# Optimization experiments

Hardware: AMD Instinct MI355X
Metric: run time of the kernel (lower is better)

Reference implementation:

```python
import jax, jax.numpy as jnp
import numpy as np

SCALE_POS = 2.0
SCALE_NEG = 40.0
THRESH_POS = 0.5
THRESH_NEG = 0.5
MARGIN = 0.1
EPS = 1e-5


def setup_inputs() -> dict:
    key = jax.random.key(0)
    kf, kl = jax.random.split(key)
    B, D, NUM_CLASSES = 4096, 1024, 64
    feats = jax.random.normal(kf, (B, D), dtype=jnp.float32)
    feats = feats / jnp.linalg.norm(feats, axis=1, keepdims=True)  # L2-normalized embeddings
    labels = jax.random.randint(kl, (B,), 0, NUM_CLASSES, dtype=jnp.int64)
    return {"feats": feats, "labels": labels}


def reference(feats, labels):
    B = feats.shape[0]
    sim = jnp.matmul(feats, feats.T)  # [B, B]
    same = labels[:, None] == labels[None, :]
    pos_mask = same & (sim < 1.0 - EPS)  # drop self / near-duplicate pairs
    neg_mask = ~same

    # hard mining: keep negatives above min positive - margin, positives below max negative + margin
    min_pos = jnp.min(jnp.where(pos_mask, sim, jnp.inf), axis=1)   # [B]
    max_neg = jnp.max(jnp.where(neg_mask, sim, -jnp.inf), axis=1)  # [B]
    neg_sel = neg_mask & (sim + MARGIN > min_pos[:, None])
    pos_sel = pos_mask & (sim - MARGIN < max_neg[:, None])

    pos_sum = jnp.sum(jnp.where(pos_sel, jnp.exp(-SCALE_POS * (sim - THRESH_POS)), 0.0), axis=1)
    neg_sum = jnp.sum(jnp.where(neg_sel, jnp.exp(SCALE_NEG * (sim - THRESH_NEG)), 0.0), axis=1)
    pos_loss = jnp.log1p(pos_sum) / SCALE_POS
    neg_loss = jnp.log1p(neg_sum) / SCALE_NEG

    valid = jnp.any(pos_sel, axis=1) & jnp.any(neg_sel, axis=1)  # rows skipped by original loop
    return jnp.sum(jnp.where(valid, pos_loss + neg_loss, 0.0)) / B
```

## Files before the change

### kernel.cpp

```cpp
#include <hip/hip_runtime.h>

typedef _Float16 half8 __attribute__((ext_vector_type(8)));
typedef float floatx4 __attribute__((ext_vector_type(4)));
typedef int intx4 __attribute__((ext_vector_type(4)));
typedef int intx8 __attribute__((ext_vector_type(8)));
typedef __attribute__((address_space(1))) const void gvoid;
typedef __attribute__((address_space(3))) void svoid;

#define SCALE_POS 2.0f
#define SCALE_NEG 40.0f
#define THRESH 0.5f
#define MARGIN 0.1f
#define EPSV 1e-5f

__device__ __forceinline__ unsigned f2ord(float f) {
    unsigned u = __float_as_uint(f);
    return (u & 0x80000000u) ? ~u : (u | 0x80000000u);
}
__device__ __forceinline__ float ord2f(unsigned e) {
    unsigned v = (e & 0x80000000u) ? (e & 0x7fffffffu) : ~e;
    return __uint_as_float(v);
}

#define ORD_POS_INF 0xff800000u
#define ORD_NEG_INF 0x007fffffu

__global__ void k_init(const float* __restrict__ feats,
                       unsigned char* __restrict__ f8,
                       unsigned* __restrict__ minp, unsigned* __restrict__ maxn,
                       float* __restrict__ psum, float* __restrict__ nsum,
                       unsigned* __restrict__ cnts,
                       int total4, int B) {
    int i = blockIdx.x * blockDim.x + threadIdx.x;
    if (i < total4) {
        float4 v = ((const float4*)feats)[i];
        int w = 0;
        w = __builtin_amdgcn_cvt_pk_fp8_f32(v.x, v.y, w, false);
        w = __builtin_amdgcn_cvt_pk_fp8_f32(v.z, v.w, w, true);
        ((int*)f8)[i] = w;
    }
    if (i < B) {
        minp[i] = ORD_POS_INF;
        maxn[i] = ORD_NEG_INF;
        psum[i] = 0.f;
        nsum[i] = 0.f;
    }
    if (i < 2048) cnts[i] = 0;
}

__global__ void __launch_bounds__(128, 2)
k_gemm_h(const unsigned char* __restrict__ f8,
         const int* __restrict__ labels,
         unsigned* __restrict__ minp_ord,
         unsigned* __restrict__ maxn_ord,
         _Float16* __restrict__ simh,
         int D, int nb) {
    __shared__ __align__(16) unsigned char As[128 * 128];
    __shared__ __align__(16) unsigned char Bs[64 * 128];
    __shared__ int labR[128], labC[64];

    const int bid = blockIdx.x;
    int t = bid >> 1;
    const int h = bid & 1;
    int rb = 0, rem = t;
    while (rem >= nb - rb) { rem -= nb - rb; ++rb; }
    const int cb = rb + rem;
    const int rowBase = rb * 128;
    const int colBase = cb * 128 + h * 64;

    const int tid = threadIdx.x;
    const int lane = tid & 63;
    const int wave = tid >> 6;
    const int q = lane >> 4;
    const int cIn = lane & 15;

    labR[tid] = labels[rowBase + tid];
    if (tid < 64) labC[tid] = labels[colBase + tid];

    const int subrow = lane >> 3;
    const int swz = (lane & 7) ^ subrow;
    const unsigned char* gP[12];
    unsigned char* lP[12];
#pragma unroll
    for (int j = 0; j < 12; ++j) {
        const int c = wave * 12 + j;
        const int grow = (c < 16) ? (rowBase + c * 8 + subrow)
                                  : (colBase + (c - 16) * 8 + subrow);
        gP[j] = f8 + (size_t)grow * D + swz * 16;
        lP[j] = ((c < 16) ? (As + c * 1024) : (Bs + (c - 16) * 1024)) + lane * 16;
    }

    int aOff0[4], aOff1[4], bOff0[4], bOff1[4];
#pragma unroll
    for (int i = 0; i < 4; ++i) {
        const int rA = wave * 64 + i * 16 + cIn;
        aOff0[i] = rA * 128 + ((2 * q) ^ (rA & 7)) * 16;
        aOff1[i] = rA * 128 + ((2 * q + 1) ^ (rA & 7)) * 16;
        const int rB = i * 16 + cIn;
        bOff0[i] = rB * 128 + ((2 * q) ^ (rB & 7)) * 16;
        bOff1[i] = rB * 128 + ((2 * q + 1) ^ (rB & 7)) * 16;
    }

    floatx4 acc[4][4] = {};

    const int KT = D >> 7;
    for (int kt = 0; kt < KT; ++kt) {
        const int kOff = kt * 128;
        __syncthreads();
#pragma unroll
        for (int j = 0; j < 12; ++j)
            __builtin_amdgcn_global_load_lds((gvoid*)(gP[j] + kOff), (svoid*)lP[j], 16, 0, 0);
        __syncthreads();

        intx8 a[4], b[4];
#pragma unroll
        for (int i = 0; i < 4; ++i) {
            intx4 lo = *(const intx4*)(As + aOff0[i]);
            intx4 hi = *(const intx4*)(As + aOff1[i]);
            a[i] = __builtin_shufflevector(lo, hi, 0, 1, 2, 3, 4, 5, 6, 7);
        }
#pragma unroll
        for (int i = 0; i < 4; ++i) {
            intx4 lo = *(const intx4*)(Bs + bOff0[i]);
            intx4 hi = *(const intx4*)(Bs + bOff1[i]);
            b[i] = __builtin_shufflevector(lo, hi, 0, 1, 2, 3, 4, 5, 6, 7);
        }
#pragma unroll
        for (int i = 0; i < 4; ++i)
#pragma unroll
            for (int j = 0; j < 4; ++j)
                acc[i][j] = __builtin_amdgcn_mfma_scale_f32_16x16x128_f8f6f4(
                    a[i], b[j], acc[i][j], 0, 0,
                    0, 0x7f7f7f7f,
                    0, 0x7f7f7f7f);
    }

    int rLabv[16];
#pragma unroll
    for (int mi = 0; mi < 4; ++mi)
#pragma unroll
        for (int rr = 0; rr < 4; ++rr)
            rLabv[mi * 4 + rr] = labR[wave * 64 + mi * 16 + q * 4 + rr];
    int cLabv[4];
#pragma unroll
    for (int ni = 0; ni < 4; ++ni)
        cLabv[ni] = labC[ni * 16 + cIn];

    {
        half8* dst = (half8*)(simh + (size_t)bid * 8192 + (size_t)tid * 64);
#pragma unroll
        for (int mi = 0; mi < 4; ++mi) {
            half8 h0, h1;
#pragma unroll
            for (int ni = 0; ni < 2; ++ni)
#pragma unroll
                for (int rr = 0; rr < 4; ++rr) {
                    h0[ni * 4 + rr] = (_Float16)acc[mi][ni][rr];
                    h1[ni * 4 + rr] = (_Float16)acc[mi][ni + 2][rr];
                }
            dst[mi * 2] = h0;
            dst[mi * 2 + 1] = h1;
        }
    }

#pragma unroll
    for (int mi = 0; mi < 4; ++mi)
#pragma unroll
        for (int rr = 0; rr < 4; ++rr) {
            const int rLoc = wave * 64 + mi * 16 + q * 4 + rr;
            const int rLab = rLabv[mi * 4 + rr];
            float vmin = 1e30f, vmax = -1e30f;
#pragma unroll
            for (int ni = 0; ni < 4; ++ni) {
                float s = acc[mi][ni][rr];
                if (rLab == cLabv[ni]) {
                    if (s < 1.0f - EPSV) vmin = fminf(vmin, s);
                } else {
                    vmax = fmaxf(vmax, s);
                }
            }
#pragma unroll
            for (int off = 8; off; off >>= 1) {
                vmin = fminf(vmin, __shfl_xor(vmin, off, 16));
                vmax = fmaxf(vmax, __shfl_xor(vmax, off, 16));
            }
            if (cIn == 0) {
                if (vmin < 1e30f) atomicMin(&minp_ord[rowBase + rLoc], f2ord(vmin));
                if (vmax > -1e30f) atomicMax(&maxn_ord[rowBase + rLoc], f2ord(vmax));
            }
        }

    if (rb != cb) {
#pragma unroll
        for (int ni = 0; ni < 4; ++ni) {
            const int cLab = cLabv[ni];
            float vmin = 1e30f, vmax = -1e30f;
#pragma unroll
            for (int mi = 0; mi < 4; ++mi)
#pragma unroll
                for (int rr = 0; rr < 4; ++rr) {
                    float s = acc[mi][ni][rr];
                    if (rLabv[mi * 4 + rr] == cLab) {
                        if (s < 1.0f - EPSV) vmin = fminf(vmin, s);
                    } else {
                        vmax = fmaxf(vmax, s);
                    }
                }
            vmin = fminf(vmin, __shfl_xor(vmin, 16, 64));
            vmin = fminf(vmin, __shfl_xor(vmin, 32, 64));
            vmax = fmaxf(vmax, __shfl_xor(vmax, 16, 64));
            vmax = fmaxf(vmax, __shfl_xor(vmax, 32, 64));
            if (q == 0) {
                const int cLoc = ni * 16 + cIn;
                if (vmin < 1e30f) atomicMin(&minp_ord[colBase + cLoc], f2ord(vmin));
                if (vmax > -1e30f) atomicMax(&maxn_ord[colBase + cLoc], f2ord(vmax));
            }
        }
    }
}

__global__ void __launch_bounds__(256)
k_sum2f(const _Float16* __restrict__ simh,
        const int* __restrict__ labels,
        const unsigned* __restrict__ minp_ord,
        const unsigned* __restrict__ maxn_ord,
        float* __restrict__ psum, float* __restrict__ nsum,
        unsigned* __restrict__ cnts,
        float* __restrict__ out,
        int nb, int B, int NT) {
    __shared__ int labR[128], labC[128];
    __shared__ float mpR[128], mnR[128], mpC[128], mnC[128];
    __shared__ float red[4];
    __shared__ unsigned lastflag;

    int t = blockIdx.x;
    int rb = 0, rem = t;
    while (rem >= nb - rb) { rem -= nb - rb; ++rb; }
    const int cb = rb + rem;
    const int rowBase = rb * 128;

    const int tid = threadIdx.x;
    const int sub = tid >> 7;
    const int stid = tid & 127;
    const int wave = stid >> 6;
    const int lane = tid & 63;
    const int q = lane >> 4;
    const int cIn = lane & 15;
    const int colBase = cb * 128 + sub * 64;

    if (tid < 128) {
        labR[tid] = labels[rowBase + tid];
        mpR[tid] = ord2f(minp_ord[rowBase + tid]) - MARGIN;
        mnR[tid] = ord2f(maxn_ord[rowBase + tid]) + MARGIN;
    } else {
        const int j = tid - 128;
        labC[j] = labels[cb * 128 + j];
        mpC[j] = ord2f(minp_ord[cb * 128 + j]) - MARGIN;
        mnC[j] = ord2f(maxn_ord[cb * 128 + j]) + MARGIN;
    }
    __syncthreads();

    int cLabv[4];
    float mpCv[4], mnCv[4];
#pragma unroll
    for (int ni = 0; ni < 4; ++ni) {
        const int j = sub * 64 + ni * 16 + cIn;
        cLabv[ni] = labC[j];
        mpCv[ni] = mpC[j];
        mnCv[ni] = mnC[j];
    }

    const half8* src = (const half8*)(simh + (size_t)(2 * t + sub) * 8192 + (size_t)stid * 64);
    half8 hv[8];
#pragma unroll
    for (int v = 0; v < 8; ++v) hv[v] = src[v];

    float cps[4] = {}, cns[4] = {};
    const bool offd = (rb != cb);

#pragma unroll
    for (int mi = 0; mi < 4; ++mi)
#pragma unroll
        for (int rr = 0; rr < 4; ++rr) {
            const int rLoc = wave * 64 + mi * 16 + q * 4 + rr;
            const int rLab = labR[rLoc];
            const float gateN = mpR[rLoc];
            const float gateP = mnR[rLoc];
            float rp = 0.f, rn = 0.f;
#pragma unroll
            for (int ni = 0; ni < 4; ++ni) {
                const int idx = mi * 16 + ni * 4 + rr;
                const float s = (float)hv[idx >> 3][idx & 7];
                if (rLab == cLabv[ni]) {
                    if (s < 1.0f - EPSV) {
                        float ev = __expf(-SCALE_POS * (s - THRESH));
                        if (s < gateP) rp += ev;
                        if (offd && s < mnCv[ni]) cps[ni] += ev;
                    }
                } else {
                    float ev = __expf(SCALE_NEG * (s - THRESH));
                    if (s > gateN) rn += ev;
                    if (offd && s > mpCv[ni]) cns[ni] += ev;
                }
            }
#pragma unroll
            for (int off = 8; off; off >>= 1) {
                rp += __shfl_xor(rp, off, 16);
                rn += __shfl_xor(rn, off, 16);
            }
            if (cIn == 0) {
                if (rp != 0.f) atomicAdd(&psum[rowBase + rLoc], rp);
                if (rn != 0.f) atomicAdd(&nsum[rowBase + rLoc], rn);
            }
        }
    if (offd) {
#pragma unroll
        for (int ni = 0; ni < 4; ++ni) {
            cps[ni] += __shfl_xor(cps[ni], 16, 64);
            cps[ni] += __shfl_xor(cps[ni], 32, 64);
            cns[ni] += __shfl_xor(cns[ni], 16, 64);
            cns[ni] += __shfl_xor(cns[ni], 32, 64);
            if (q == 0) {
                const int cLoc = ni * 16 + cIn;
                if (cps[ni] != 0.f) atomicAdd(&psum[colBase + cLoc], cps[ni]);
                if (cns[ni] != 0.f) atomicAdd(&nsum[colBase + cLoc], cns[ni]);
            }
        }
    }

    __syncthreads();
    if (tid == 0) {
        const unsigned stripe = (unsigned)blockIdx.x & 31u;
        const unsigned stripe_target = (unsigned)((NT - (int)stripe + 31) / 32);
        unsigned prev = __hip_atomic_fetch_add(&cnts[(1 + stripe) * 32], 1u,
                                               __ATOMIC_RELAXED, __HIP_MEMORY_SCOPE_AGENT);
        unsigned lf = 0u;
        if (prev == stripe_target - 1u) {
            unsigned ptop = __hip_atomic_fetch_add(&cnts[0], 1u,
                                                   __ATOMIC_RELAXED, __HIP_MEMORY_SCOPE_AGENT);
            lf = (ptop == 31u) ? 1u : 0u;
        }
        lastflag = lf;
    }
    __syncthreads();
    if (lastflag) {
        float a = 0.f;
        for (int i = tid; i < B; i += 256) {
            float pv = atomicAdd(&psum[i], 0.0f);
            float nv = atomicAdd(&nsum[i], 0.0f);
            if (pv > 0.f && nv > 0.f)
                a += log1pf(pv) * (1.0f / SCALE_POS) + log1pf(nv) * (1.0f / SCALE_NEG);
        }
#pragma unroll
        for (int off = 32; off; off >>= 1) a += __shfl_down(a, off, 64);
        if ((tid & 63) == 0) red[tid >> 6] = a;
        __syncthreads();
        if (tid == 0) out[0] = (red[0] + red[1] + red[2] + red[3]) / (float)B;
    }
}

extern "C" void kernel_launch(void* const* d_in, const int* in_sizes, int n_in,
                              void* d_out, int out_size, void* d_ws, size_t ws_size,
                              hipStream_t stream) {
    const float* feats = (const float*)d_in[0];
    const int* labels = (const int*)d_in[1];
    const int B = in_sizes[1];
    const int D = in_sizes[0] / B;
    const int nb = B / 128;
    const int NT = nb * (nb + 1) / 2;
    const int NH = NT * 2;
    const int total4 = B * D / 4;

    char* ws = (char*)d_ws;
    unsigned char* f8 = (unsigned char*)ws;
    size_t off = (size_t)B * D;
    unsigned* minp = (unsigned*)(ws + off); off += (size_t)B * 4;
    unsigned* maxn = (unsigned*)(ws + off); off += (size_t)B * 4;
    float* psum = (float*)(ws + off); off += (size_t)B * 4;
    float* nsum = (float*)(ws + off); off += (size_t)B * 4;
    unsigned* cnts = (unsigned*)(ws + off); off += 8192;
    _Float16* simh = (_Float16*)(ws + ((off + 255) & ~(size_t)255));
    float* outp = (float*)d_out;

    k_init<<<(total4 + 255) / 256, 256, 0, stream>>>(feats, f8, minp, maxn,
                                                     psum, nsum, cnts, total4, B);

    k_gemm_h<<<NH, 128, 0, stream>>>(f8, labels, minp, maxn, simh, D, nb);

    k_sum2f<<<NT, 256, 0, stream>>>(simh, labels, minp, maxn, psum, nsum,
                                    cnts, outp, nb, B, NT);
}
```

Baseline: 136.9 us.

## Double-buffer LDS tiles to overlap global loads with MFMA compute

Measured after the change: 138.9 us. About the same (+1.4%).

```diff
diff --git a/kernel.cpp b/kernel.cpp
--- a/kernel.cpp
+++ b/kernel.cpp
@@ -55,8 +55,7 @@
          unsigned* __restrict__ maxn_ord,
          _Float16* __restrict__ simh,
          int D, int nb) {
-    __shared__ __align__(16) unsigned char As[128 * 128];
-    __shared__ __align__(16) unsigned char Bs[64 * 128];
+    __shared__ __align__(16) unsigned char S[2][24 * 1024];
     __shared__ int labR[128], labC[64];
 
     const int bid = blockIdx.x;
@@ -87,7 +86,7 @@
         const int grow = (c < 16) ? (rowBase + c * 8 + subrow)
                                   : (colBase + (c - 16) * 8 + subrow);
         gP[j] = f8 + (size_t)grow * D + swz * 16;
-        lP[j] = ((c < 16) ? (As + c * 1024) : (Bs + (c - 16) * 1024)) + lane * 16;
+        lP[j] = S[0] + c * 1024 + lane * 16;
     }
 
     int aOff0[4], aOff1[4], bOff0[4], bOff1[4];
@@ -97,43 +96,62 @@
         aOff0[i] = rA * 128 + ((2 * q) ^ (rA & 7)) * 16;
         aOff1[i] = rA * 128 + ((2 * q + 1) ^ (rA & 7)) * 16;
         const int rB = i * 16 + cIn;
-        bOff0[i] = rB * 128 + ((2 * q) ^ (rB & 7)) * 16;
-        bOff1[i] = rB * 128 + ((2 * q + 1) ^ (rB & 7)) * 16;
+        bOff0[i] = 16384 + rB * 128 + ((2 * q) ^ (rB & 7)) * 16;
+        bOff1[i] = 16384 + rB * 128 + ((2 * q + 1) ^ (rB & 7)) * 16;
     }
 
     floatx4 acc[4][4] = {};
 
+#define STAGE(buf, kOff)                                                       \
+    {                                                                          \
+        _Pragma("unroll")                                                      \
+        for (int j = 0; j < 12; ++j)                                           \
+            __builtin_amdgcn_global_load_lds((gvoid*)(gP[j] + (kOff)),         \
+                                             (svoid*)(lP[j] + (buf) * 24576), \
+                                             16, 0, 0);                        \
+    }
+
+#define COMPUTE(buf)                                                           \
+    {                                                                          \
+        const unsigned char* Sb = S[0] + (buf) * 24576;                        \
+        intx8 a[4], b[4];                                                      \
+        _Pragma("unroll")                                                      \
+        for (int i = 0; i < 4; ++i) {                                          \
+            intx4 lo = *(const intx4*)(Sb + aOff0[i]);                         \
+            intx4 hi = *(const intx4*)(Sb + aOff1[i]);                         \
+            a[i] = __builtin_shufflevector(lo, hi, 0, 1, 2, 3, 4, 5, 6, 7);    \
+        }                                                                      \
+        _Pragma("unroll")                                                      \
+        for (int i = 0; i < 4; ++i) {                                          \
+            intx4 lo = *(const intx4*)(Sb + bOff0[i]);                         \
+            intx4 hi = *(const intx4*)(Sb + bOff1[i]);                         \
+            b[i] = __builtin_shufflevector(lo, hi, 0, 1, 2, 3, 4, 5, 6, 7);    \
+        }                                                                      \
+        _Pragma("unroll")                                                      \
+        for (int i = 0; i < 4; ++i)                                            \
+            _Pragma("unroll")                                                  \
+            for (int j2 = 0; j2 < 4; ++j2)                                     \
+                acc[i][j2] = __builtin_amdgcn_mfma_scale_f32_16x16x128_f8f6f4( \
+                    a[i], b[j2], acc[i][j2], 0, 0,                             \
+                    0, 0x7f7f7f7f, 0, 0x7f7f7f7f);                             \
+    }
+
     const int KT = D >> 7;
-    for (int kt = 0; kt < KT; ++kt) {
-        const int kOff = kt * 128;
+
+    STAGE(0, 0);
+    __syncthreads();
+
+    for (int kt = 0; kt < KT; kt += 2) {
+        if (kt + 1 < KT) STAGE(1, (kt + 1) << 7);
+        COMPUTE(0);
         __syncthreads();
-#pragma unroll
-        for (int j = 0; j < 12; ++j)
-            __builtin_amdgcn_global_load_lds((gvoid*)(gP[j] + kOff), (svoid*)lP[j], 16, 0, 0);
+        if (kt + 2 < KT) STAGE(0, (kt + 2) << 7);
+        COMPUTE(1);
         __syncthreads();
-
-        intx8 a[4], b[4];
-#pragma unroll
-        for (int i = 0; i < 4; ++i) {
-            intx4 lo = *(const intx4*)(As + aOff0[i]);
-            intx4 hi = *(const intx4*)(As + aOff1[i]);
-            a[i] = __builtin_shufflevector(lo, hi, 0, 1, 2, 3, 4, 5, 6, 7);
-        }
-#pragma unroll
-        for (int i = 0; i < 4; ++i) {
-            intx4 lo = *(const intx4*)(Bs + bOff0[i]);
-            intx4 hi = *(const intx4*)(Bs + bOff1[i]);
-            b[i] = __builtin_shufflevector(lo, hi, 0, 1, 2, 3, 4, 5, 6, 7);
-        }
-#pragma unroll
-        for (int i = 0; i < 4; ++i)
-#pragma unroll
-            for (int j = 0; j < 4; ++j)
-                acc[i][j] = __builtin_amdgcn_mfma_scale_f32_16x16x128_f8f6f4(
-                    a[i], b[j], acc[i][j], 0, 0,
-                    0, 0x7f7f7f7f,
-                    0, 0x7f7f7f7f);
-    }
+    }
+
+#undef STAGE
+#undef COMPUTE
 
     int rLabv[16];
 #pragma unroll
```

## Merge half-tile GEMM blocks into full 128x128 tiles with 4 waves and XCD-aware remap

Applied to the files above, without the earlier changes.

Measured after the change: 138.5 us. Within noise of the previous version (+1.1%).

```diff
diff --git a/kernel.cpp b/kernel.cpp
--- a/kernel.cpp
+++ b/kernel.cpp
@@ -48,7 +48,7 @@
     if (i < 2048) cnts[i] = 0;
 }
 
-__global__ void __launch_bounds__(128, 2)
+__global__ void __launch_bounds__(256, 4)
 k_gemm_h(const unsigned char* __restrict__ f8,
          const int* __restrict__ labels,
          unsigned* __restrict__ minp_ord,
@@ -56,34 +56,35 @@
          _Float16* __restrict__ simh,
          int D, int nb) {
     __shared__ __align__(16) unsigned char As[128 * 128];
-    __shared__ __align__(16) unsigned char Bs[64 * 128];
-    __shared__ int labR[128], labC[64];
-
-    const int bid = blockIdx.x;
-    int t = bid >> 1;
-    const int h = bid & 1;
+    __shared__ __align__(16) unsigned char Bs[128 * 128];
+    __shared__ int labR[128], labC[128];
+
+    const int bid0 = blockIdx.x;
+    const int t = (bid0 & 7) * 66 + (bid0 >> 3);
     int rb = 0, rem = t;
     while (rem >= nb - rb) { rem -= nb - rb; ++rb; }
     const int cb = rb + rem;
     const int rowBase = rb * 128;
-    const int colBase = cb * 128 + h * 64;
+    const int colBase = cb * 128;
 
     const int tid = threadIdx.x;
     const int lane = tid & 63;
     const int wave = tid >> 6;
+    const int wr = wave >> 1;
+    const int wc = wave & 1;
     const int q = lane >> 4;
     const int cIn = lane & 15;
 
-    labR[tid] = labels[rowBase + tid];
-    if (tid < 64) labC[tid] = labels[colBase + tid];
+    if (tid < 128) labR[tid] = labels[rowBase + tid];
+    else           labC[tid - 128] = labels[colBase + (tid - 128)];
 
     const int subrow = lane >> 3;
     const int swz = (lane & 7) ^ subrow;
-    const unsigned char* gP[12];
-    unsigned char* lP[12];
-#pragma unroll
-    for (int j = 0; j < 12; ++j) {
-        const int c = wave * 12 + j;
+    const unsigned char* gP[8];
+    unsigned char* lP[8];
+#pragma unroll
+    for (int j = 0; j < 8; ++j) {
+        const int c = wave * 8 + j;
         const int grow = (c < 16) ? (rowBase + c * 8 + subrow)
                                   : (colBase + (c - 16) * 8 + subrow);
         gP[j] = f8 + (size_t)grow * D + swz * 16;
@@ -93,10 +94,10 @@
     int aOff0[4], aOff1[4], bOff0[4], bOff1[4];
 #pragma unroll
     for (int i = 0; i < 4; ++i) {
-        const int rA = wave * 64 + i * 16 + cIn;
+        const int rA = wr * 64 + i * 16 + cIn;
         aOff0[i] = rA * 128 + ((2 * q) ^ (rA & 7)) * 16;
         aOff1[i] = rA * 128 + ((2 * q + 1) ^ (rA & 7)) * 16;
-        const int rB = i * 16 + cIn;
+        const int rB = wc * 64 + i * 16 + cIn;
         bOff0[i] = rB * 128 + ((2 * q) ^ (rB & 7)) * 16;
         bOff1[i] = rB * 128 + ((2 * q + 1) ^ (rB & 7)) * 16;
     }
@@ -108,7 +109,7 @@
         const int kOff = kt * 128;
         __syncthreads();
 #pragma unroll
-        for (int j = 0; j < 12; ++j)
+        for (int j = 0; j < 8; ++j)
             __builtin_amdgcn_global_load_lds((gvoid*)(gP[j] + kOff), (svoid*)lP[j], 16, 0, 0);
         __syncthreads();
 
@@ -128,9 +129,9 @@
 #pragma unroll
         for (int i = 0; i < 4; ++i)
 #pragma unroll
-            for (int j = 0; j < 4; ++j)
-                acc[i][j] = __builtin_amdgcn_mfma_scale_f32_16x16x128_f8f6f4(
-                    a[i], b[j], acc[i][j], 0, 0,
+            for (int j2 = 0; j2 < 4; ++j2)
+                acc[i][j2] = __builtin_amdgcn_mfma_scale_f32_16x16x128_f8f6f4(
+                    a[i], b[j2], acc[i][j2], 0, 0,
                     0, 0x7f7f7f7f,
                     0, 0x7f7f7f7f);
     }
@@ -140,14 +141,15 @@
     for (int mi = 0; mi < 4; ++mi)
 #pragma unroll
         for (int rr = 0; rr < 4; ++rr)
-            rLabv[mi * 4 + rr] = labR[wave * 64 + mi * 16 + q * 4 + rr];
+            rLabv[mi * 4 + rr] = labR[wr * 64 + mi * 16 + q * 4 + rr];
     int cLabv[4];
 #pragma unroll
     for (int ni = 0; ni < 4; ++ni)
-        cLabv[ni] = labC[ni * 16 + cIn];
+        cLabv[ni] = labC[wc * 64 + ni * 16 + cIn];
 
     {
-        half8* dst = (half8*)(simh + (size_t)bid * 8192 + (size_t)tid * 64);
+        half8* dst = (half8*)(simh + (size_t)(2 * t + wc) * 8192
+                                   + (size_t)(wr * 64 + lane) * 64);
 #pragma unroll
         for (int mi = 0; mi < 4; ++mi) {
             half8 h0, h1;
@@ -167,7 +169,7 @@
     for (int mi = 0; mi < 4; ++mi)
 #pragma unroll
         for (int rr = 0; rr < 4; ++rr) {
-            const int rLoc = wave * 64 + mi * 16 + q * 4 + rr;
+            const int rLoc = wr * 64 + mi * 16 + q * 4 + rr;
             const int rLab = rLabv[mi * 4 + rr];
             float vmin = 1e30f, vmax = -1e30f;
 #pragma unroll
@@ -211,7 +213,7 @@
             vmax = fmaxf(vmax, __shfl_xor(vmax, 16, 64));
             vmax = fmaxf(vmax, __shfl_xor(vmax, 32, 64));
             if (q == 0) {
-                const int cLoc = ni * 16 + cIn;
+                const int cLoc = wc * 64 + ni * 16 + cIn;
                 if (vmin < 1e30f) atomicMin(&minp_ord[colBase + cLoc], f2ord(vmin));
                 if (vmax > -1e30f) atomicMax(&maxn_ord[colBase + cLoc], f2ord(vmax));
             }
@@ -368,7 +370,6 @@
     const int D = in_sizes[0] / B;
     const int nb = B / 128;
     const int NT = nb * (nb + 1) / 2;
-    const int NH = NT * 2;
     const int total4 = B * D / 4;
 
     char* ws = (char*)d_ws;
@@ -385,7 +386,7 @@
     k_init<<<(total4 + 255) / 256, 256, 0, stream>>>(feats, f8, minp, maxn,
                                                      psum, nsum, cnts, total4, B);
 
-    k_gemm_h<<<NH, 128, 0, stream>>>(f8, labels, minp, maxn, simh, D, nb);
+    k_gemm_h<<<NT, 256, 0, stream>>>(f8, labels, minp, maxn, simh, D, nb);
 
     k_sum2f<<<NT, 256, 0, stream>>>(simh, labels, minp, maxn, psum, nsum,
                                     cnts, outp, nb, B, NT);
```
